# Performance work log

Hardware: AMD Instinct MI355X
Metric: run time of the kernel (lower is better)

## Reference

```python
import jax, jax.numpy as jnp
import numpy as np

N, C, B, HF, WF, HID = 200000, 128, 4, 116, 200, 64
STRIDE = 8
MAX_BEV_RANGE = 72.0
LN_EPS = 1e-5


def setup_inputs() -> dict:
    key = jax.random.key(0)
    ks = jax.random.split(key, 20)
    s = 0.05  # weight scale
    x = jax.random.normal(ks[0], (N, C), jnp.float32)
    # sparse voxel indices: (batch, z, y, x) on a 128x128x5 stride-8 grid
    bi = jax.random.randint(ks[1], (N, 1), 0, B)
    zi = jax.random.randint(ks[2], (N, 1), 0, 5)
    yi = jax.random.randint(ks[3], (N, 1), 0, 128)
    xi = jax.random.randint(ks[4], (N, 1), 0, 128)
    indices = jnp.concatenate([bi, zi, yi, xi], axis=1).astype(jnp.int32)
    voxel_size = jnp.array([0.1, 0.1, 0.2], jnp.float32)
    pc_range = jnp.array([-51.2, -51.2, -5.0, 51.2, 51.2, 3.0], jnp.float32)
    # plausible lidar->image projection: cam_x=-y, cam_y=-z, cam_z=x, K=[1000,800;1000,450]
    Rt = np.array([[0.0, -1.0, 0.0, 0.0],
                   [0.0, 0.0, -1.0, 1.6],
                   [1.0, 0.0, 0.0, 0.0]], np.float32)
    K = np.array([[1000.0, 0.0, 800.0], [0.0, 1000.0, 450.0], [0.0, 0.0, 1.0]], np.float32)
    P = K @ Rt  # [3,4]
    trans = jnp.asarray(np.tile(P[None], (B, 1, 1)))
    trans = trans + 0.01 * jax.random.normal(ks[5], (B, 3, 4), jnp.float32)
    img_feats = jax.random.normal(ks[6], (B, C, HF, WF), jnp.float32)
    return {
        'x': x, 'indices': indices, 'voxel_size': voxel_size, 'pc_range': pc_range,
        'trans_lidar_to_img': trans, 'img_feats': img_feats, 'img_h': 928, 'img_w': 1600,
        'fg_w1': s * jax.random.normal(ks[7], (C, HID)), 'fg_b1': jnp.zeros((HID,)),
        'fg_w2': s * jax.random.normal(ks[8], (HID, 1)), 'fg_b2': jnp.zeros((1,)),
        'rt_w1': s * jax.random.normal(ks[9], (C + 3, HID)), 'rt_b1': jnp.zeros((HID,)),
        'rt_w2': s * jax.random.normal(ks[10], (HID, 3)),
        'rt_b2': jnp.array([2.0, 0.0, -1.0], jnp.float32),
        'le_w1': s * jax.random.normal(ks[11], (2 * C, C)), 'le_b1': jnp.zeros((C,)),
        'le_w2': s * jax.random.normal(ks[12], (C, C)), 'le_b2': jnp.zeros((C,)),
        'ln_g': jnp.ones((C,)), 'ln_b': jnp.zeros((C,)),
    }


def _bilinear_sample(img_t, b, u_norm, v_norm):
    # img_t: [B,H,W,C]; grid_sample bilinear, align_corners=True, padding_mode='zeros'
    Hf, Wf = img_t.shape[1], img_t.shape[2]
    px = (u_norm + 1.0) * 0.5 * (Wf - 1)
    py = (v_norm + 1.0) * 0.5 * (Hf - 1)
    x0 = jnp.floor(px)
    y0 = jnp.floor(py)
    fx, fy = px - x0, py - y0
    x0i, y0i = x0.astype(jnp.int32), y0.astype(jnp.int32)
    out = jnp.zeros((px.shape[0], img_t.shape[-1]), img_t.dtype)
    for dy in (0, 1):
        for dx in (0, 1):
            xi, yi = x0i + dx, y0i + dy
            w = (fx if dx else 1.0 - fx) * (fy if dy else 1.0 - fy)
            inb = (xi >= 0) & (xi < Wf) & (yi >= 0) & (yi < Hf)
            f = img_t[b, jnp.clip(yi, 0, Hf - 1), jnp.clip(xi, 0, Wf - 1)]
            out = out + f * (w * inb.astype(w.dtype))[:, None]
    return out


def _layernorm(h, g, b):
    mu = jnp.mean(h, axis=-1, keepdims=True)
    var = jnp.mean(jnp.square(h - mu), axis=-1, keepdims=True)
    return (h - mu) * jax.lax.rsqrt(var + LN_EPS) * g + b


def reference(x, indices, voxel_size, pc_range, trans_lidar_to_img, img_feats,
              img_h, img_w, fg_w1, fg_b1, fg_w2, fg_b2, rt_w1, rt_b1, rt_w2, rt_b2,
              le_w1, le_b1, le_w2, le_b2, ln_g, ln_b):
    # voxel centers: indices[:,1:]=(z,y,x) -> (x,y,z)
    spatial = indices[:, 1:][:, ::-1].astype(jnp.float32)
    cvs = voxel_size * STRIDE
    centers = spatial * cvs + pc_range[:3] + cvs / 2.0  # [N,3]
    range_norm = jnp.linalg.norm(centers[:, :2], axis=-1, keepdims=True)
    range_norm = jnp.clip(range_norm / max(MAX_BEV_RANGE, 1e-6), 0.0, 1.0)

    # project to image plane
    ones = jnp.ones((centers.shape[0], 1), centers.dtype)
    xyz_hom = jnp.concatenate([centers, ones], axis=1)  # [N,4]
    batch_ids = indices[:, 0]
    P = trans_lidar_to_img[batch_ids]  # [N,3,4]
    pts = jnp.einsum('nij,nj->ni', P, xyz_hom)
    depth = pts[:, 2]
    safe = jnp.maximum(depth, 1e-5)
    u_feat = pts[:, 0] / safe * (float(WF) / float(img_w))
    v_feat = pts[:, 1] / safe * (float(HF) / float(img_h))
    u_norm = 2.0 * (u_feat / max(WF - 1, 1)) - 1.0
    v_norm = 2.0 * (v_feat / max(HF - 1, 1)) - 1.0
    valid = (depth > 1e-5) & (jnp.abs(u_norm) <= 1.0) & (jnp.abs(v_norm) <= 1.0)
    valid_f = valid.astype(jnp.float32)[:, None]  # [N,1]

    # router
    p_fg = jax.nn.sigmoid(jax.nn.relu(x @ fg_w1 + fg_b1) @ fg_w2 + fg_b2)  # [N,1]
    rin = jnp.concatenate([x, range_norm, p_fg, valid_f], axis=-1)
    route_weights = jax.nn.softmax(jax.nn.relu(rin @ rt_w1 + rt_b1) @ rt_w2 + rt_b2, axis=-1)

    # per-point grid_sample gather from image features
    img_t = jnp.transpose(img_feats, (0, 2, 3, 1))  # [B,H,W,C]
    sampled = _bilinear_sample(img_t, batch_ids, u_norm, v_norm)  # [N,C]

    # light fusion expert
    h = jnp.concatenate([x, sampled], axis=-1)
    delta_light = (jax.nn.relu(h @ le_w1 + le_b1) @ le_w2 + le_b2) * valid_f
    delta = route_weights[:, 1:2] * delta_light  # rectified expert disabled (RECTIFY_RATIO=0)

    fusion_gain = jnp.linalg.norm(delta, axis=-1, keepdims=True) / (
        jnp.linalg.norm(x, axis=-1, keepdims=True) + 1e-6)
    fusion_gain = jnp.clip(1.0 - jnp.exp(-fusion_gain), 0.0, 1.0)

    fused = _layernorm(x + delta, ln_g, ln_b)  # [N,C]

    zeros1 = jnp.zeros_like(p_fg)
    quality = jnp.clip(jnp.concatenate(
        [route_weights, p_fg, range_norm, valid_f, zeros1, fusion_gain,
         zeros1, zeros1, zeros1], axis=-1), 0.0, 1.0)  # [N,11]
    return fused, quality
```

## Files before the change

kernel.cpp:

```cpp
#include <hip/hip_runtime.h>

namespace {

typedef __attribute__((ext_vector_type(8))) short bf16x8;
typedef __attribute__((ext_vector_type(4))) float f32x4;

constexpr int C     = 128;
constexpr int HF    = 116;
constexpr int WF    = 200;
constexpr int PTILE = 32;
constexpr int BLK   = 256;
constexpr int NPTS  = 200000;
constexpr int AS_STRIDE  = 264;
constexpr int HID_STRIDE = 136;

constexpr int W_LE1 = 0;
constexpr int W_LE2 = 32768;
constexpr int W_FG  = 49152;
constexpr int W_RT  = 57344;
constexpr size_t IMG_BYTE_OFF = 131072;

constexpr int IMG_BLOCKS = 4 * HF * 2;
constexpr int WP_BLOCKS  = 256;

__device__ __forceinline__ float b2f(unsigned short u) {
  union { unsigned int i; float f; } v; v.i = ((unsigned int)u) << 16; return v.f;
}
__device__ __forceinline__ unsigned short f2b(float f) {
  union { float f; unsigned int i; } v; v.f = f;
  unsigned int i = v.i;
  return (unsigned short)((i + 0x7fffu + ((i >> 16) & 1u)) >> 16);
}
__device__ __forceinline__ void unp(unsigned int u, float& lo, float& hi) {
  union { unsigned int i; float f; } a, b;
  a.i = u << 16; b.i = u & 0xffff0000u; lo = a.f; hi = b.f;
}
__device__ __forceinline__ unsigned int packb(float a, float b) {
  unsigned int r;
  asm("v_cvt_pk_bf16_f32 %0, %1, %2" : "=v"(r) : "v"(a), "v"(b));
  return r;
}

__global__ __launch_bounds__(BLK) void prep_kernel(
    const float* __restrict__ imgf,
    const float* __restrict__ le_w1, const float* __restrict__ le_w2,
    const float* __restrict__ fg_w1, const float* __restrict__ rt_w1,
    short* __restrict__ wpack, short* __restrict__ imgT) {
  __shared__ short buf[100 * HID_STRIDE];
  const int blk = blockIdx.x;
  if (blk < IMG_BLOCKS) {
    const int half = blk & 1, by = blk >> 1;
    const int b = by / HF, y = by - b * HF;
    const int x0 = half * 100;
    const float* s = imgf + (size_t)b * C * HF * WF + (size_t)y * WF + x0;
    for (int i = threadIdx.x; i < C * 25; i += BLK) {
      int c = i / 25, qx = i - c * 25;
      float4 v = *(const float4*)(s + (size_t)c * (HF * WF) + qx * 4);
      int xb = qx * 4;
      buf[(xb + 0) * HID_STRIDE + c] = (short)f2b(v.x);
      buf[(xb + 1) * HID_STRIDE + c] = (short)f2b(v.y);
      buf[(xb + 2) * HID_STRIDE + c] = (short)f2b(v.z);
      buf[(xb + 3) * HID_STRIDE + c] = (short)f2b(v.w);
    }
    __syncthreads();
    short* d = imgT + ((size_t)(b * HF + y) * WF + x0) * C;
    for (int i = threadIdx.x; i < 100 * 16; i += BLK) {
      int xx = i >> 4, c8 = (i & 15) << 3;
      *(uint4*)(d + (size_t)xx * C + c8) = *(const uint4*)&buf[xx * HID_STRIDE + c8];
    }
  } else {
    int idx = (blk - IMG_BLOCKS) * BLK + threadIdx.x;
    if (idx < 32768) {
      int k = idx >> 7, n = idx & 127;
      wpack[W_LE1 + (((k >> 3) * 128 + n) << 3) + (k & 7)] = (short)f2b(le_w1[idx]);
    } else if (idx < 49152) {
      int l = idx - 32768; int k = l >> 7, n = l & 127;
      wpack[W_LE2 + (((k >> 3) * 128 + n) << 3) + (k & 7)] = (short)f2b(le_w2[l]);
    } else if (idx < 57344) {
      int l = idx - 49152; int k = l >> 6, n = l & 63;
      wpack[W_FG + (((k >> 3) * 64 + n) << 3) + (k & 7)] = (short)f2b(fg_w1[l]);
    } else {
      int l = idx - 57344; int k = l >> 6, n = l & 63;
      wpack[W_RT + (((k >> 3) * 64 + n) << 3) + (k & 7)] = (short)f2b(rt_w1[k * 64 + n]);
    }
  }
}

__global__ __launch_bounds__(BLK, 6) void fuse_kernel(
    const float* __restrict__ x,
    const int*   __restrict__ indices,
    const float* __restrict__ vox, const float* __restrict__ pcr,
    const float* __restrict__ trans,
    const int* __restrict__ imgh_p, const int* __restrict__ imgw_p,
    const float* __restrict__ fg_b1v, const float* __restrict__ fg_w2v,
    const float* __restrict__ fg_b2v,
    const float* __restrict__ rt_w1f,
    const float* __restrict__ rt_b1v, const float* __restrict__ rt_w2v,
    const float* __restrict__ rt_b2v,
    const float* __restrict__ le_b1v, const float* __restrict__ le_b2v,
    const float* __restrict__ ln_gv, const float* __restrict__ ln_bv,
    const short* __restrict__ wpack,
    const short* __restrict__ imgT,
    float* __restrict__ out_fused, float* __restrict__ out_qual) {
  __shared__ short As[PTILE * AS_STRIDE];
  __shared__ float s_rn[32], s_pfg[32], s_valid[32], s_px[32], s_py[32];
  __shared__ float s_gain[32], s_rv[32];
  __shared__ float s_route[32][3];
  __shared__ int   s_bat[32];
  __shared__ __align__(16) float s_lnpart[4][16][4];

  const int tid  = threadIdx.x;
  const int n0   = blockIdx.x * PTILE;
  const int wave = tid >> 6;
  const int lane = tid & 63;
  const int q    = lane >> 4;
  const int nn   = lane & 15;

  {
    const float4* xsrc = (const float4*)(x + (size_t)n0 * C);
    for (int i = tid; i < PTILE * C / 4; i += BLK) {
      float4 v = xsrc[i];
      int p = i >> 5, c4 = (i & 31) * 4;
      uint2 sv = { packb(v.x, v.y), packb(v.z, v.w) };
      *(uint2*)&As[p * AS_STRIDE + c4] = sv;
    }
  }
  if (tid < PTILE) {
    int p = tid;
    int base = (n0 + p) * 4;
    int bi = indices[base + 0], zi = indices[base + 1];
    int yi = indices[base + 2], xi = indices[base + 3];
    float sp[3] = { (float)xi, (float)yi, (float)zi };
    float cen[3];
#pragma unroll
    for (int k = 0; k < 3; ++k) {
      float cvs = vox[k] * 8.0f;
      cen[k] = sp[k] * cvs + pcr[k] + cvs * 0.5f;
    }
    float rn = sqrtf(cen[0] * cen[0] + cen[1] * cen[1]) / 72.0f;
    rn = fminf(fmaxf(rn, 0.0f), 1.0f);
    float pt3[3];
#pragma unroll
    for (int r = 0; r < 3; ++r) {
      const float* row = trans + (bi * 3 + r) * 4;
      pt3[r] = row[0] * cen[0] + row[1] * cen[1] + row[2] * cen[2] + row[3];
    }
    float depth = pt3[2];
    float safe  = fmaxf(depth, 1e-5f);
    float uf = pt3[0] / safe * ((float)WF / (float)imgw_p[0]);
    float vf = pt3[1] / safe * ((float)HF / (float)imgh_p[0]);
    float un = 2.0f * (uf / (float)(WF - 1)) - 1.0f;
    float vn = 2.0f * (vf / (float)(HF - 1)) - 1.0f;
    bool valid = (depth > 1e-5f) && (fabsf(un) <= 1.0f) && (fabsf(vn) <= 1.0f);
    s_rn[p] = rn;
    s_valid[p] = valid ? 1.0f : 0.0f;
    s_bat[p] = bi;
    s_px[p] = (un + 1.0f) * 0.5f * (float)(WF - 1);
    s_py[p] = (vn + 1.0f) * 0.5f * (float)(HF - 1);
  }
  __syncthreads();

  f32x4 accS[4];
#pragma unroll
  for (int t = 0; t < 4; ++t) accS[t] = (f32x4){0.f, 0.f, 0.f, 0.f};
  if (wave < 2) {
    const int p0 = wave * 16;
    const bf16x8* Bfg = (const bf16x8*)(wpack + W_FG);
#pragma unroll 2
    for (int ks = 0; ks < 4; ++ks) {
      bf16x8 a = *(const bf16x8*)&As[(p0 + nn) * AS_STRIDE + ks * 32 + q * 8];
#pragma unroll
      for (int t = 0; t < 4; ++t) {
        bf16x8 b = Bfg[(ks * 4 + q) * 64 + t * 16 + nn];
        accS[t] = __builtin_amdgcn_mfma_f32_16x16x32_bf16(a, b, accS[t], 0, 0, 0);
      }
    }
    float part[4] = {0.f, 0.f, 0.f, 0.f};
#pragma unroll
    for (int t = 0; t < 4; ++t) {
      int col = t * 16 + nn;
      float bias = fg_b1v[col];
      float wv2  = fg_w2v[col];
#pragma unroll
      for (int r = 0; r < 4; ++r)
        part[r] += fmaxf(accS[t][r] + bias, 0.f) * wv2;
    }
#pragma unroll
    for (int off = 1; off < 16; off <<= 1) {
#pragma unroll
      for (int r = 0; r < 4; ++r) part[r] += __shfl_xor(part[r], off);
    }
    if (nn == 0) {
      float b2 = fg_b2v[0];
#pragma unroll
      for (int r = 0; r < 4; ++r)
        s_pfg[p0 + q * 4 + r] = 1.f / (1.f + expf(-(part[r] + b2)));
    }
  } else {
    const int p0 = (wave - 2) * 16;
    const bf16x8* Brt = (const bf16x8*)(wpack + W_RT);
#pragma unroll 2
    for (int ks = 0; ks < 4; ++ks) {
      bf16x8 a = *(const bf16x8*)&As[(p0 + nn) * AS_STRIDE + ks * 32 + q * 8];
#pragma unroll
      for (int t = 0; t < 4; ++t) {
        bf16x8 b = Brt[(ks * 4 + q) * 64 + t * 16 + nn];
        accS[t] = __builtin_amdgcn_mfma_f32_16x16x32_bf16(a, b, accS[t], 0, 0, 0);
      }
    }
  }
  __syncthreads();

  if (wave >= 2) {
    const int p0 = (wave - 2) * 16;
    float lg0[4] = {0,0,0,0}, lg1[4] = {0,0,0,0}, lg2[4] = {0,0,0,0};
#pragma unroll
    for (int t = 0; t < 4; ++t) {
      int col = t * 16 + nn;
      float b1 = rt_b1v[col];
      float wr = rt_w1f[128 * 64 + col];
      float wp = rt_w1f[129 * 64 + col];
      float wv = rt_w1f[130 * 64 + col];
      float w20 = rt_w2v[col * 3 + 0], w21 = rt_w2v[col * 3 + 1], w22 = rt_w2v[col * 3 + 2];
#pragma unroll
      for (int r = 0; r < 4; ++r) {
        int p = p0 + q * 4 + r;
        float h = accS[t][r] + b1 + s_rn[p] * wr + s_pfg[p] * wp + s_valid[p] * wv;
        h = fmaxf(h, 0.f);
        lg0[r] += h * w20; lg1[r] += h * w21; lg2[r] += h * w22;
      }
    }
#pragma unroll
    for (int off = 1; off < 16; off <<= 1) {
#pragma unroll
      for (int r = 0; r < 4; ++r) {
        lg0[r] += __shfl_xor(lg0[r], off);
        lg1[r] += __shfl_xor(lg1[r], off);
        lg2[r] += __shfl_xor(lg2[r], off);
      }
    }
    if (nn == 0) {
      float rb0 = rt_b2v[0], rb1 = rt_b2v[1], rb2 = rt_b2v[2];
#pragma unroll
      for (int r = 0; r < 4; ++r) {
        int p = p0 + q * 4 + r;
        float l0 = lg0[r] + rb0, l1 = lg1[r] + rb1, l2 = lg2[r] + rb2;
        float m = fmaxf(l0, fmaxf(l1, l2));
        float e0 = expf(l0 - m), e1 = expf(l1 - m), e2 = expf(l2 - m);
        float inv = 1.f / (e0 + e1 + e2);
        s_route[p][0] = e0 * inv; s_route[p][1] = e1 * inv; s_route[p][2] = e2 * inv;
        s_rv[p] = e1 * inv * s_valid[p];
      }
    }
  }
  {
    int p = tid >> 3, grp = tid & 7, ch0 = grp * 16;
    float sacc[16];
#pragma unroll
    for (int k = 0; k < 16; ++k) sacc[k] = 0.f;
    if (s_valid[p] > 0.5f) {
      float px = s_px[p], py = s_py[p];
      float x0f = floorf(px), y0f = floorf(py);
      float fx = px - x0f, fy = py - y0f;
      int ix = (int)x0f, iy = (int)y0f;
      int bb = s_bat[p];
#pragma unroll
      for (int dy = 0; dy < 2; ++dy) {
#pragma unroll
        for (int dx = 0; dx < 2; ++dx) {
          int xi = ix + dx, yi = iy + dy;
          if (xi >= 0 && xi < WF && yi >= 0 && yi < HF) {
            float w = (dx ? fx : 1.0f - fx) * (dy ? fy : 1.0f - fy);
            const short* tp = imgT + (((size_t)bb * HF + yi) * WF + xi) * C + ch0;
            uint4 u0 = *(const uint4*)tp;
            uint4 u1 = *(const uint4*)(tp + 8);
            float lo, hi;
            unp(u0.x, lo, hi); sacc[0] += w * lo;  sacc[1] += w * hi;
            unp(u0.y, lo, hi); sacc[2] += w * lo;  sacc[3] += w * hi;
            unp(u0.z, lo, hi); sacc[4] += w * lo;  sacc[5] += w * hi;
            unp(u0.w, lo, hi); sacc[6] += w * lo;  sacc[7] += w * hi;
            unp(u1.x, lo, hi); sacc[8] += w * lo;  sacc[9] += w * hi;
            unp(u1.y, lo, hi); sacc[10] += w * lo; sacc[11] += w * hi;
            unp(u1.z, lo, hi); sacc[12] += w * lo; sacc[13] += w * hi;
            unp(u1.w, lo, hi); sacc[14] += w * lo; sacc[15] += w * hi;
          }
        }
      }
    }
    uint4 o0 = { packb(sacc[0], sacc[1]),  packb(sacc[2], sacc[3]),
                 packb(sacc[4], sacc[5]),  packb(sacc[6], sacc[7]) };
    uint4 o1 = { packb(sacc[8], sacc[9]),  packb(sacc[10], sacc[11]),
                 packb(sacc[12], sacc[13]), packb(sacc[14], sacc[15]) };
    *(uint4*)&As[p * AS_STRIDE + 128 + ch0]     = o0;
    *(uint4*)&As[p * AS_STRIDE + 128 + ch0 + 8] = o1;
  }
  __syncthreads();

  {
    const bf16x8* Ble1 = (const bf16x8*)(wpack + W_LE1);
    f32x4 acc[2][2];
#pragma unroll
    for (int rg = 0; rg < 2; ++rg)
#pragma unroll
      for (int t2 = 0; t2 < 2; ++t2) acc[rg][t2] = (f32x4){0.f, 0.f, 0.f, 0.f};
#pragma unroll 2
    for (int ks = 0; ks < 8; ++ks) {
      bf16x8 b0 = Ble1[(ks * 4 + q) * 128 + (wave * 2 + 0) * 16 + nn];
      bf16x8 b1 = Ble1[(ks * 4 + q) * 128 + (wave * 2 + 1) * 16 + nn];
#pragma unroll
      for (int rg = 0; rg < 2; ++rg) {
        bf16x8 a = *(const bf16x8*)&As[(rg * 16 + nn) * AS_STRIDE + ks * 32 + q * 8];
        acc[rg][0] = __builtin_amdgcn_mfma_f32_16x16x32_bf16(a, b0, acc[rg][0], 0, 0, 0);
        acc[rg][1] = __builtin_amdgcn_mfma_f32_16x16x32_bf16(a, b1, acc[rg][1], 0, 0, 0);
      }
    }
    __syncthreads();
#pragma unroll
    for (int t2 = 0; t2 < 2; ++t2) {
      int col = (wave * 2 + t2) * 16 + nn;
      float bias = le_b1v[col];
#pragma unroll
      for (int rg = 0; rg < 2; ++rg)
#pragma unroll
        for (int r = 0; r < 4; ++r)
          As[(rg * 16 + q * 4 + r) * AS_STRIDE + 128 + col] =
              (short)f2b(fmaxf(acc[rg][t2][r] + bias, 0.f));
    }
    __syncthreads();
  }

  const int pt = wave & 1, cg = wave >> 1;
  const int p0le = pt * 16;
  const bf16x8* Ble2 = (const bf16x8*)(wpack + W_LE2);
  f32x4 acc2[4];
#pragma unroll
  for (int t = 0; t < 4; ++t) acc2[t] = (f32x4){0.f, 0.f, 0.f, 0.f};
#pragma unroll 2
  for (int ks = 0; ks < 4; ++ks) {
    bf16x8 a = *(const bf16x8*)&As[(p0le + nn) * AS_STRIDE + 128 + ks * 32 + q * 8];
#pragma unroll
    for (int t = 0; t < 4; ++t) {
      bf16x8 b = Ble2[(ks * 4 + q) * 128 + (cg * 4 + t) * 16 + nn];
      acc2[t] = __builtin_amdgcn_mfma_f32_16x16x32_bf16(a, b, acc2[t], 0, 0, 0);
    }
  }
  float yv[4][4];
  float psum[4] = {0,0,0,0}, psum2[4] = {0,0,0,0}, pd2[4] = {0,0,0,0}, px2[4] = {0,0,0,0};
#pragma unroll
  for (int t = 0; t < 4; ++t) {
    int col = (cg * 4 + t) * 16 + nn;
    float bias = le_b2v[col];
#pragma unroll
    for (int r = 0; r < 4; ++r) {
      int p = p0le + q * 4 + r;
      float d  = (acc2[t][r] + bias) * s_rv[p];
      float xv = b2f((unsigned short)As[p * AS_STRIDE + col]);
      float y  = xv + d;
      yv[t][r] = y;
      psum[r]  += y;       psum2[r] += y * y;
      pd2[r]   += d * d;   px2[r]   += xv * xv;
    }
  }
#pragma unroll
  for (int off = 1; off < 16; off <<= 1) {
#pragma unroll
    for (int r = 0; r < 4; ++r) {
      psum[r]  += __shfl_xor(psum[r], off);
      psum2[r] += __shfl_xor(psum2[r], off);
      pd2[r]   += __shfl_xor(pd2[r], off);
      px2[r]   += __shfl_xor(px2[r], off);
    }
  }
  if (nn == 0) {
#pragma unroll
    for (int r = 0; r < 4; ++r) {
      f32x4 st = { psum[r], psum2[r], pd2[r], px2[r] };
      *(f32x4*)&s_lnpart[wave][q * 4 + r][0] = st;
    }
  }
  __syncthreads();
  {
    float gcol[4], bcol[4];
#pragma unroll
    for (int t = 0; t < 4; ++t) {
      int col = (cg * 4 + t) * 16 + nn;
      gcol[t] = ln_gv[col]; bcol[t] = ln_bv[col];
    }
#pragma unroll
    for (int r = 0; r < 4; ++r) {
      int lr = q * 4 + r;
      int p  = p0le + lr;
      f32x4 oth = *(const f32x4*)&s_lnpart[wave ^ 2][lr][0];
      float sy  = psum[r]  + oth[0];
      float sy2 = psum2[r] + oth[1];
      float sd2 = pd2[r]   + oth[2];
      float sx2 = px2[r]   + oth[3];
      float mu  = sy * (1.f / 128.f);
      float var = sy2 * (1.f / 128.f) - mu * mu;
      float inv = rsqrtf(var + 1e-5f);
      if (wave < 2 && nn == 0) {
        float gain = sqrtf(sd2) / (sqrtf(sx2) + 1e-6f);
        s_gain[p] = fminf(fmaxf(1.f - expf(-gain), 0.f), 1.f);
      }
      float* orow = out_fused + (size_t)(n0 + p) * C;
#pragma unroll
      for (int t = 0; t < 4; ++t) {
        int col = (cg * 4 + t) * 16 + nn;
        orow[col] = (yv[t][r] - mu) * inv * gcol[t] + bcol[t];
      }
    }
  }
  __syncthreads();

  for (int idx = tid; idx < PTILE * 11; idx += BLK) {
    int p2 = idx / 11, k = idx - p2 * 11;
    float v = 0.0f;
    if (k < 3)       v = s_route[p2][k];
    else if (k == 3) v = s_pfg[p2];
    else if (k == 4) v = s_rn[p2];
    else if (k == 5) v = s_valid[p2];
    else if (k == 7) v = s_gain[p2];
    v = fminf(fmaxf(v, 0.0f), 1.0f);
    out_qual[(size_t)(n0 + p2) * 11 + k] = v;
  }
}

}

extern "C" void kernel_launch(void* const* d_in, const int* in_sizes, int n_in,
                              void* d_out, int out_size, void* d_ws, size_t ws_size,
                              hipStream_t stream) {
  const float* x       = (const float*)d_in[0];
  const int*   indices = (const int*)d_in[1];
  const float* vox     = (const float*)d_in[2];
  const float* pcr     = (const float*)d_in[3];
  const float* trans   = (const float*)d_in[4];
  const float* imgf    = (const float*)d_in[5];
  const int*   imgh    = (const int*)d_in[6];
  const int*   imgw    = (const int*)d_in[7];
  const float* fg_w1   = (const float*)d_in[8];
  const float* fg_b1   = (const float*)d_in[9];
  const float* fg_w2   = (const float*)d_in[10];
  const float* fg_b2   = (const float*)d_in[11];
  const float* rt_w1   = (const float*)d_in[12];
  const float* rt_b1   = (const float*)d_in[13];
  const float* rt_w2   = (const float*)d_in[14];
  const float* rt_b2   = (const float*)d_in[15];
  const float* le_w1   = (const float*)d_in[16];
  const float* le_b1   = (const float*)d_in[17];
  const float* le_w2   = (const float*)d_in[18];
  const float* le_b2   = (const float*)d_in[19];
  const float* ln_g    = (const float*)d_in[20];
  const float* ln_b    = (const float*)d_in[21];

  short* wpack = (short*)d_ws;
  short* imgT  = (short*)((char*)d_ws + IMG_BYTE_OFF);

  float* out_fused = (float*)d_out;
  float* out_qual  = out_fused + (size_t)NPTS * C;

  (void)in_sizes; (void)n_in; (void)out_size; (void)ws_size;

  prep_kernel<<<IMG_BLOCKS + WP_BLOCKS, BLK, 0, stream>>>(
      imgf, le_w1, le_w2, fg_w1, rt_w1, wpack, imgT);
  fuse_kernel<<<NPTS / PTILE, BLK, 0, stream>>>(
      x, indices, vox, pcr, trans, imgh, imgw,
      fg_b1, fg_w2, fg_b2,
      rt_w1, rt_b1, rt_w2, rt_b2,
      le_b1, le_b2, ln_g, ln_b,
      wpack, imgT, out_fused, out_qual);
}
```

Baseline: 335.0 us.

## Double point tile to 64 with 512-thread blocks and remap wave work split

Doubles the point tile of the fuse kernel from 32 to 64 and the block size from 256 to 512 threads (8 waves). The wave-to-work mapping for the fg/route, light-expert first-layer and second-layer GEMMs and the LayerNorm partial exchange is reassigned to match. Each loaded weight fragment is now reused across more points, and per-block fixed overhead is spread over more points. The prep kernel keeps 256 threads through a separate constant. In exchange, shared memory per block grows, and the tighter launch bound may cap registers and cause spills or lower occupancy.

```diff
diff --git a/kernel.cpp b/kernel.cpp
--- a/kernel.cpp
+++ b/kernel.cpp
@@ -8,8 +8,8 @@
 constexpr int C     = 128;
 constexpr int HF    = 116;
 constexpr int WF    = 200;
-constexpr int PTILE = 32;
-constexpr int BLK   = 256;
+constexpr int PTILE = 64;
+constexpr int BLK   = 512;
 constexpr int NPTS  = 200000;
 constexpr int AS_STRIDE  = 264;
 constexpr int HID_STRIDE = 136;
@@ -20,6 +20,7 @@
 constexpr int W_RT  = 57344;
 constexpr size_t IMG_BYTE_OFF = 131072;
 
+constexpr int PREP_BLK   = 256;
 constexpr int IMG_BLOCKS = 4 * HF * 2;
 constexpr int WP_BLOCKS  = 256;
 
@@ -41,7 +42,7 @@
   return r;
 }
 
-__global__ __launch_bounds__(BLK) void prep_kernel(
+__global__ __launch_bounds__(PREP_BLK) void prep_kernel(
     const float* __restrict__ imgf,
     const float* __restrict__ le_w1, const float* __restrict__ le_w2,
     const float* __restrict__ fg_w1, const float* __restrict__ rt_w1,
@@ -53,7 +54,7 @@
     const int b = by / HF, y = by - b * HF;
     const int x0 = half * 100;
     const float* s = imgf + (size_t)b * C * HF * WF + (size_t)y * WF + x0;
-    for (int i = threadIdx.x; i < C * 25; i += BLK) {
+    for (int i = threadIdx.x; i < C * 25; i += PREP_BLK) {
       int c = i / 25, qx = i - c * 25;
       float4 v = *(const float4*)(s + (size_t)c * (HF * WF) + qx * 4);
       int xb = qx * 4;
@@ -64,12 +65,12 @@
     }
     __syncthreads();
     short* d = imgT + ((size_t)(b * HF + y) * WF + x0) * C;
-    for (int i = threadIdx.x; i < 100 * 16; i += BLK) {
+    for (int i = threadIdx.x; i < 100 * 16; i += PREP_BLK) {
       int xx = i >> 4, c8 = (i & 15) << 3;
       *(uint4*)(d + (size_t)xx * C + c8) = *(const uint4*)&buf[xx * HID_STRIDE + c8];
     }
   } else {
-    int idx = (blk - IMG_BLOCKS) * BLK + threadIdx.x;
+    int idx = (blk - IMG_BLOCKS) * PREP_BLK + threadIdx.x;
     if (idx < 32768) {
       int k = idx >> 7, n = idx & 127;
       wpack[W_LE1 + (((k >> 3) * 128 + n) << 3) + (k & 7)] = (short)f2b(le_w1[idx]);
@@ -86,7 +87,7 @@
   }
 }
 
-__global__ __launch_bounds__(BLK, 6) void fuse_kernel(
+__global__ __launch_bounds__(BLK, 8) void fuse_kernel(
     const float* __restrict__ x,
     const int*   __restrict__ indices,
     const float* __restrict__ vox, const float* __restrict__ pcr,
@@ -103,11 +104,11 @@
     const short* __restrict__ imgT,
     float* __restrict__ out_fused, float* __restrict__ out_qual) {
   __shared__ short As[PTILE * AS_STRIDE];
-  __shared__ float s_rn[32], s_pfg[32], s_valid[32], s_px[32], s_py[32];
-  __shared__ float s_gain[32], s_rv[32];
-  __shared__ float s_route[32][3];
-  __shared__ int   s_bat[32];
-  __shared__ __align__(16) float s_lnpart[4][16][4];
+  __shared__ float s_rn[64], s_pfg[64], s_valid[64], s_px[64], s_py[64];
+  __shared__ float s_gain[64], s_rv[64];
+  __shared__ float s_route[64][3];
+  __shared__ int   s_bat[64];
+  __shared__ __align__(16) float s_lnpart[8][16][4];
 
   const int tid  = threadIdx.x;
   const int n0   = blockIdx.x * PTILE;
@@ -163,7 +164,7 @@
   f32x4 accS[4];
 #pragma unroll
   for (int t = 0; t < 4; ++t) accS[t] = (f32x4){0.f, 0.f, 0.f, 0.f};
-  if (wave < 2) {
+  if (wave < 4) {
     const int p0 = wave * 16;
     const bf16x8* Bfg = (const bf16x8*)(wpack + W_FG);
 #pragma unroll 2
@@ -197,7 +198,7 @@
         s_pfg[p0 + q * 4 + r] = 1.f / (1.f + expf(-(part[r] + b2)));
     }
   } else {
-    const int p0 = (wave - 2) * 16;
+    const int p0 = (wave - 4) * 16;
     const bf16x8* Brt = (const bf16x8*)(wpack + W_RT);
 #pragma unroll 2
     for (int ks = 0; ks < 4; ++ks) {
@@ -211,8 +212,8 @@
   }
   __syncthreads();
 
-  if (wave >= 2) {
-    const int p0 = (wave - 2) * 16;
+  if (wave >= 4) {
+    const int p0 = (wave - 4) * 16;
     float lg0[4] = {0,0,0,0}, lg1[4] = {0,0,0,0}, lg2[4] = {0,0,0,0};
 #pragma unroll
     for (int t = 0; t < 4; ++t) {
@@ -298,39 +299,35 @@
 
   {
     const bf16x8* Ble1 = (const bf16x8*)(wpack + W_LE1);
-    f32x4 acc[2][2];
-#pragma unroll
-    for (int rg = 0; rg < 2; ++rg)
-#pragma unroll
-      for (int t2 = 0; t2 < 2; ++t2) acc[rg][t2] = (f32x4){0.f, 0.f, 0.f, 0.f};
+    f32x4 acc[4];
+#pragma unroll
+    for (int rg = 0; rg < 4; ++rg) acc[rg] = (f32x4){0.f, 0.f, 0.f, 0.f};
 #pragma unroll 2
     for (int ks = 0; ks < 8; ++ks) {
-      bf16x8 b0 = Ble1[(ks * 4 + q) * 128 + (wave * 2 + 0) * 16 + nn];
-      bf16x8 b1 = Ble1[(ks * 4 + q) * 128 + (wave * 2 + 1) * 16 + nn];
-#pragma unroll
-      for (int rg = 0; rg < 2; ++rg) {
+      bf16x8 b = Ble1[(ks * 4 + q) * 128 + wave * 16 + nn];
+#pragma unroll
+      for (int rg = 0; rg < 4; ++rg) {
         bf16x8 a = *(const bf16x8*)&As[(rg * 16 + nn) * AS_STRIDE + ks * 32 + q * 8];
-        acc[rg][0] = __builtin_amdgcn_mfma_f32_16x16x32_bf16(a, b0, acc[rg][0], 0, 0, 0);
-        acc[rg][1] = __builtin_amdgcn_mfma_f32_16x16x32_bf16(a, b1, acc[rg][1], 0, 0, 0);
+        acc[rg] = __builtin_amdgcn_mfma_f32_16x16x32_bf16(a, b, acc[rg], 0, 0, 0);
       }
     }
     __syncthreads();
-#pragma unroll
-    for (int t2 = 0; t2 < 2; ++t2) {
-      int col = (wave * 2 + t2) * 16 + nn;
+    {
+      int col = wave * 16 + nn;
       float bias = le_b1v[col];
 #pragma unroll
-      for (int rg = 0; rg < 2; ++rg)
+      for (int rg = 0; rg < 4; ++rg)
 #pragma unroll
         for (int r = 0; r < 4; ++r)
           As[(rg * 16 + q * 4 + r) * AS_STRIDE + 128 + col] =
-              (short)f2b(fmaxf(acc[rg][t2][r] + bias, 0.f));
+              (short)f2b(fmaxf(acc[rg][r] + bias, 0.f));
     }
     __syncthreads();
   }
 
-  const int pt = wave & 1, cg = wave >> 1;
-  const int p0le = pt * 16;
+  const int rq  = wave >> 1;
+  const int chh = wave & 1;
+  const int p0le = rq * 16;
   const bf16x8* Ble2 = (const bf16x8*)(wpack + W_LE2);
   f32x4 acc2[4];
 #pragma unroll
@@ -340,7 +337,7 @@
     bf16x8 a = *(const bf16x8*)&As[(p0le + nn) * AS_STRIDE + 128 + ks * 32 + q * 8];
 #pragma unroll
     for (int t = 0; t < 4; ++t) {
-      bf16x8 b = Ble2[(ks * 4 + q) * 128 + (cg * 4 + t) * 16 + nn];
+      bf16x8 b = Ble2[(ks * 4 + q) * 128 + (chh * 4 + t) * 16 + nn];
       acc2[t] = __builtin_amdgcn_mfma_f32_16x16x32_bf16(a, b, acc2[t], 0, 0, 0);
     }
   }
@@ -348,7 +345,7 @@
   float psum[4] = {0,0,0,0}, psum2[4] = {0,0,0,0}, pd2[4] = {0,0,0,0}, px2[4] = {0,0,0,0};
 #pragma unroll
   for (int t = 0; t < 4; ++t) {
-    int col = (cg * 4 + t) * 16 + nn;
+    int col = (chh * 4 + t) * 16 + nn;
     float bias = le_b2v[col];
 #pragma unroll
     for (int r = 0; r < 4; ++r) {
@@ -383,14 +380,14 @@
     float gcol[4], bcol[4];
 #pragma unroll
     for (int t = 0; t < 4; ++t) {
-      int col = (cg * 4 + t) * 16 + nn;
+      int col = (chh * 4 + t) * 16 + nn;
       gcol[t] = ln_gv[col]; bcol[t] = ln_bv[col];
     }
 #pragma unroll
     for (int r = 0; r < 4; ++r) {
       int lr = q * 4 + r;
       int p  = p0le + lr;
-      f32x4 oth = *(const f32x4*)&s_lnpart[wave ^ 2][lr][0];
+      f32x4 oth = *(const f32x4*)&s_lnpart[wave ^ 1][lr][0];
       float sy  = psum[r]  + oth[0];
       float sy2 = psum2[r] + oth[1];
       float sd2 = pd2[r]   + oth[2];
@@ -398,14 +395,14 @@
       float mu  = sy * (1.f / 128.f);
       float var = sy2 * (1.f / 128.f) - mu * mu;
       float inv = rsqrtf(var + 1e-5f);
-      if (wave < 2 && nn == 0) {
+      if (chh == 0 && nn == 0) {
         float gain = sqrtf(sd2) / (sqrtf(sx2) + 1e-6f);
         s_gain[p] = fminf(fmaxf(1.f - expf(-gain), 0.f), 1.f);
       }
       float* orow = out_fused + (size_t)(n0 + p) * C;
 #pragma unroll
       for (int t = 0; t < 4; ++t) {
-        int col = (cg * 4 + t) * 16 + nn;
+        int col = (chh * 4 + t) * 16 + nn;
         orow[col] = (yv[t][r] - mu) * inv * gcol[t] + bcol[t];
       }
     }
@@ -461,7 +458,7 @@
 
   (void)in_sizes; (void)n_in; (void)out_size; (void)ws_size;
 
-  prep_kernel<<<IMG_BLOCKS + WP_BLOCKS, BLK, 0, stream>>>(
+  prep_kernel<<<IMG_BLOCKS + WP_BLOCKS, PREP_BLK, 0, stream>>>(
       imgf, le_w1, le_w2, fg_w1, rt_w1, wpack, imgT);
   fuse_kernel<<<NPTS / PTILE, BLK, 0, stream>>>(
       x, indices, vox, pcr, trans, imgh, imgw,
```

After: 333.3 us. Within noise of the previous version (-0.5%).
